# Kernel tuning notes

Hardware: AMD Instinct MI355X
Metric: run time of the kernel (lower is better)

The kernel has to match this reference:

```python
import jax, jax.numpy as jnp
import numpy as np

N_ENTITY = 100000
H_DIM = 512
N_ROWS = 262144
ALPHA = 0.5          # EMA rate for fast state
GATE_TH = 0.5        # gate_threshold buffer
GATE_SCALE = 5.0     # gate_scale buffer
LN_EPS = 1e-5


def setup_inputs() -> dict:
    key = jax.random.key(0)
    k1, k2, k3, k4, k5 = jax.random.split(key, 5)
    entity_emb = jax.random.normal(k1, (N_ROWS, H_DIM), dtype=jnp.float32)
    entity_ids = jax.random.randint(k2, (N_ROWS,), 0, N_ENTITY, dtype=jnp.int64)
    slow_state = 0.1 * jax.random.normal(k3, (N_ENTITY, H_DIM), dtype=jnp.float32)
    fast_state = 0.1 * jax.random.normal(k4, (N_ENTITY, H_DIM), dtype=jnp.float32)
    # torch nn.Linear(2h, h): weight shape (h, 2h), y = x @ W.T + b
    W = jax.random.normal(k5, (H_DIM, 2 * H_DIM), dtype=jnp.float32) * 0.02
    b = jnp.zeros((H_DIM,), dtype=jnp.float32)
    return {"entity_emb": entity_emb, "slow_state": slow_state,
            "fast_state": fast_state, "W": W, "b": b, "entity_ids": entity_ids}


def _layer_norm(x):
    mu = jnp.mean(x, axis=-1, keepdims=True)
    var = jnp.mean(jnp.square(x - mu), axis=-1, keepdims=True)
    return (x - mu) * jax.lax.rsqrt(var + LN_EPS)


def reference(entity_emb, slow_state, fast_state, W, b, entity_ids):
    # ---- fuse_with_state (gate path) ----
    state = slow_state[entity_ids]                                   # (N, h) gather
    is_active = (jnp.sum(jnp.abs(state), axis=-1, keepdims=True) > 1e-6).astype(entity_emb.dtype)
    h_state = _layer_norm(state)
    gate_in = jnp.concatenate([entity_emb, h_state], axis=-1)        # (N, 2h)
    z = jax.nn.sigmoid(gate_in @ W.T + b)                            # (N, h)
    fused = z * entity_emb + (1.0 - z) * h_state
    out = is_active * fused + (1.0 - is_active) * entity_emb

    # ---- writeback (no-grad in torch; scatter-reduce EMA + norm-gated slow update) ----
    ctx = jax.lax.stop_gradient(out)
    ids = entity_ids
    counts = jax.ops.segment_sum(jnp.ones((ctx.shape[0],), ctx.dtype), ids,
                                 num_segments=N_ENTITY)              # (E,)
    ctx_sum = jax.ops.segment_sum(ctx, ids, num_segments=N_ENTITY)   # (E, h)
    ctx_mean = ctx_sum / jnp.clip(counts, 1.0)[:, None]
    touched = (counts > 0)[:, None]
    new_fast_all = (1.0 - ALPHA) * fast_state + ALPHA * ctx_mean
    new_fast = jnp.where(touched, new_fast_all, fast_state)
    diff = new_fast - slow_state
    delta = jnp.linalg.norm(diff, axis=-1, keepdims=True)
    gate = jax.nn.sigmoid(GATE_SCALE * (delta - GATE_TH))
    new_slow = jnp.where(touched, slow_state + gate * diff, slow_state)
    return out, new_fast, new_slow
```

## Files before the change

### kernel.cpp

```cpp
#include <hip/hip_runtime.h>
#include <hip/hip_bf16.h>
#include <cstdint>

#define NROWS 262144
#define HDIM  512
#define NENT  100000
#define SCAN_NBLK ((NENT + 1023) / 1024)

typedef __attribute__((ext_vector_type(4))) float  f32x4;
typedef __attribute__((ext_vector_type(8))) short  bf16x8;
typedef __attribute__((ext_vector_type(4))) short  bf16x4;

static __device__ __forceinline__ unsigned short f2bf(float x) {
    unsigned u = __float_as_uint(x);
    u += 0x7FFF + ((u >> 16) & 1);
    return (unsigned short)(u >> 16);
}
static __device__ __forceinline__ float bf2f(unsigned short h) {
    return __uint_as_float(((unsigned)h) << 16);
}

__global__ void pack_w_kernel(const float* __restrict__ W,
                              unsigned short* __restrict__ WeP,
                              unsigned short* __restrict__ WsP) {
    int g    = blockIdx.x * 256 + threadIdx.x;
    int sel  = g >> 15;
    int gg   = g & 32767;
    int lane = gg & 63;
    int ct   = (gg >> 6) & 3;
    int kt   = (gg >> 8) & 15;
    int w    = gg >> 12;
    int col  = (w * 4 + ct) * 16 + (lane & 15);
    int k    = kt * 32 + ((lane >> 4) << 3) + sel * 512;
    const float* src = W + (size_t)col * 1024 + k;
    f32x4 v0 = *(const f32x4*)(src);
    f32x4 v1 = *(const f32x4*)(src + 4);
    bf16x8 ov;
#pragma unroll
    for (int i = 0; i < 4; ++i) {
        ov[i]     = (short)f2bf(v0[i]);
        ov[4 + i] = (short)f2bf(v1[i]);
    }
    unsigned short* dst = sel ? WsP : WeP;
    *(bf16x8*)(dst + (size_t)gg * 8) = ov;
}

__global__ __launch_bounds__(256) void zero_kernel(unsigned* __restrict__ p) {
    int i = blockIdx.x * 256 + threadIdx.x;
    if (i < NENT) p[i] = 0u;
}

__global__ __launch_bounds__(256) void count_kernel(const int* __restrict__ ids,
                                                    unsigned* __restrict__ counts) {
    int r = blockIdx.x * 256 + threadIdx.x;
    if (r < NROWS) atomicAdd(&counts[ids[r]], 1u);
}

__global__ __launch_bounds__(1024) void scan1_kernel(const unsigned* __restrict__ counts,
                                                     unsigned* __restrict__ off,
                                                     unsigned* __restrict__ bsums) {
    __shared__ unsigned tmp[1024];
    int i = blockIdx.x * 1024 + threadIdx.x;
    unsigned v = (i < NENT) ? counts[i] : 0u;
    tmp[threadIdx.x] = v;
    __syncthreads();
#pragma unroll
    for (int o = 1; o < 1024; o <<= 1) {
        unsigned a = (threadIdx.x >= o) ? tmp[threadIdx.x - o] : 0u;
        __syncthreads();
        tmp[threadIdx.x] += a;
        __syncthreads();
    }
    if (i < NENT) off[i] = tmp[threadIdx.x] - v;
    if (threadIdx.x == 1023) bsums[blockIdx.x] = tmp[1023];
}

__global__ void scan2_kernel(unsigned* __restrict__ bsums) {
    if (threadIdx.x == 0 && blockIdx.x == 0) {
        unsigned s = 0;
        for (int i = 0; i < SCAN_NBLK; ++i) { unsigned t = bsums[i]; bsums[i] = s; s += t; }
    }
}

__global__ __launch_bounds__(1024) void scan3_kernel(unsigned* __restrict__ off,
                                                     const unsigned* __restrict__ bsums,
                                                     unsigned* __restrict__ cursor) {
    int i = blockIdx.x * 1024 + threadIdx.x;
    if (i < NENT) {
        unsigned o = off[i] + bsums[blockIdx.x];
        off[i] = o;
        cursor[i] = o;
    }
    if (i == 0) off[NENT] = NROWS;
}

__global__ __launch_bounds__(256) void fill_kernel(const int* __restrict__ ids,
                                                   unsigned* __restrict__ cursor,
                                                   int* __restrict__ rowidx) {
    int r = blockIdx.x * 256 + threadIdx.x;
    if (r < NROWS) {
        unsigned p = atomicAdd(&cursor[ids[r]], 1u);
        rowidx[p] = r;
    }
}

__global__ __launch_bounds__(512, 4) void entity_kernel(
    const float* __restrict__ slow, const unsigned short* __restrict__ WsP,
    const float* __restrict__ bias, unsigned short* __restrict__ hB,
    unsigned short* __restrict__ GsB, float* __restrict__ actB)
{
    __shared__ unsigned short xLds[2048 * 8];
    __shared__ float muS[32], rsS[32], bS[512];

    const int t    = threadIdx.x;
    const int w    = t >> 6;
    const int lane = t & 63;
    const int brow = blockIdx.x * 32;

    if (t < 128) ((f32x4*)bS)[t] = ((const f32x4*)bias)[t];

    for (int rr = 0; rr < 4; ++rr) {
        int row = w * 4 + rr;
        int e   = brow + row;
        const float* sp = slow + (size_t)e * HDIM;
        f32x4 v0 = ((const f32x4*)sp)[lane * 2];
        f32x4 v1 = ((const f32x4*)sp)[lane * 2 + 1];
        float s = 0.f, s2 = 0.f, sa = 0.f;
#pragma unroll
        for (int i = 0; i < 4; ++i) {
            s  += v0[i] + v1[i];
            s2 += v0[i] * v0[i] + v1[i] * v1[i];
            sa += fabsf(v0[i]) + fabsf(v1[i]);
        }
#pragma unroll
        for (int m = 32; m >= 1; m >>= 1) {
            s  += __shfl_xor(s, m);
            s2 += __shfl_xor(s2, m);
            sa += __shfl_xor(sa, m);
        }
        if (lane == 0) {
            float mu  = s * (1.f / HDIM);
            float var = s2 * (1.f / HDIM) - mu * mu;
            muS[row] = mu;
            rsS[row] = rsqrtf(var + 1e-5f);
            actB[e]  = (sa > 1e-6f) ? 1.f : 0.f;
        }
    }
    __syncthreads();

#pragma unroll
    for (int i = 0; i < 4; ++i) {
        int s  = t + i * 512;
        int T  = s >> 6, ls = s & 63;
        int row = (T & 1) * 16 + (ls & 15);
        int k   = (T >> 1) * 32 + ((ls >> 4) << 3);
        const float* p = slow + (size_t)(brow + row) * HDIM + k;
        f32x4 x0 = *(const f32x4*)p, x1 = *(const f32x4*)(p + 4);
        float mu = muS[row], rs = rsS[row];
        bf16x8 av;
#pragma unroll
        for (int j = 0; j < 4; ++j) {
            av[j]     = (short)f2bf((x0[j] - mu) * rs);
            av[4 + j] = (short)f2bf((x1[j] - mu) * rs);
        }
        ((bf16x8*)xLds)[s] = av;
    }
    __syncthreads();

    f32x4 zero4 = {0.f, 0.f, 0.f, 0.f};
    f32x4 acc[2][4];
#pragma unroll
    for (int i = 0; i < 2; ++i)
#pragma unroll
        for (int j = 0; j < 4; ++j) acc[i][j] = zero4;

    const unsigned short* wpW = WsP + (size_t)w * 32768 + (size_t)lane * 8;

#define LOADW(dst, kt)                                                  \
    {   _Pragma("unroll")                                               \
        for (int ct = 0; ct < 4; ++ct)                                  \
            dst[ct] = *(const bf16x8*)(wpW + ((kt) * 4 + ct) * 512);    \
    }
#define LOADX(dst, kt)                                                  \
    {   _Pragma("unroll")                                               \
        for (int rt = 0; rt < 2; ++rt)                                  \
            dst[rt] = ((const bf16x8*)xLds)[((kt) * 2 + rt) * 64 + lane]; \
    }
#define STEP(wf, xf)                                                    \
    {   _Pragma("unroll")                                               \
        for (int ct = 0; ct < 4; ++ct) {                                \
            acc[0][ct] = __builtin_amdgcn_mfma_f32_16x16x32_bf16(wf[ct], xf[0], acc[0][ct], 0, 0, 0); \
            acc[1][ct] = __builtin_amdgcn_mfma_f32_16x16x32_bf16(wf[ct], xf[1], acc[1][ct], 0, 0, 0); \
        }                                                               \
    }

    {
        bf16x8 wA[4], wB[4], xA[2], xB[2];
        LOADW(wA, 0); LOADX(xA, 0);
#pragma unroll
        for (int kt = 0; kt < 16; kt += 2) {
            if (kt + 1 < 16) { LOADW(wB, kt + 1); LOADX(xB, kt + 1); }
            STEP(wA, xA);
            if (kt + 2 < 16) { LOADW(wA, kt + 2); LOADX(xA, kt + 2); }
            if (kt + 1 < 16) STEP(wB, xB);
        }
    }

#pragma unroll
    for (int rt = 0; rt < 2; ++rt) {
        int e = brow + rt * 16 + (lane & 15);
#pragma unroll
        for (int ct = 0; ct < 4; ++ct) {
            int col0 = w * 64 + ct * 16 + ((lane >> 4) << 2);
            f32x4 bv = *(const f32x4*)&bS[col0];
            bf16x4 gv;
#pragma unroll
            for (int r = 0; r < 4; ++r) gv[r] = (short)f2bf(acc[rt][ct][r] + bv[r]);
            *(bf16x4*)(GsB + (size_t)e * HDIM + col0) = gv;
        }
    }
#pragma unroll
    for (int i = 0; i < 4; ++i) {
        int s  = t + i * 512;
        int T  = s >> 6, ls = s & 63;
        int row = (T & 1) * 16 + (ls & 15);
        int k   = (T >> 1) * 32 + ((ls >> 4) << 3);
        *(bf16x8*)(hB + (size_t)(brow + row) * HDIM + k) = ((const bf16x8*)xLds)[s];
    }
}

__global__ __launch_bounds__(512, 4) void fuse_kernel(
    const float* __restrict__ emb, const unsigned short* __restrict__ WeP,
    const int* __restrict__ ids, const unsigned short* __restrict__ hB,
    const unsigned short* __restrict__ GsB, const float* __restrict__ actB,
    float* __restrict__ out)
{
    __shared__ unsigned short xLds[2048 * 8];
    __shared__ int idS[32];

    const int t    = threadIdx.x;
    const int w    = t >> 6;
    const int lane = t & 63;
    const int brow = blockIdx.x * 32;

    if (t < 32) idS[t] = ids[brow + t];

#pragma unroll
    for (int i = 0; i < 4; ++i) {
        int s  = t + i * 512;
        int T  = s >> 6, ls = s & 63;
        int row = (T & 1) * 16 + (ls & 15);
        int k   = (T >> 1) * 32 + ((ls >> 4) << 3);
        const float* p = emb + (size_t)(brow + row) * HDIM + k;
        f32x4 x0 = *(const f32x4*)p, x1 = *(const f32x4*)(p + 4);
        bf16x8 av;
#pragma unroll
        for (int j = 0; j < 4; ++j) {
            av[j]     = (short)f2bf(x0[j]);
            av[4 + j] = (short)f2bf(x1[j]);
        }
        ((bf16x8*)xLds)[s] = av;
    }
    __syncthreads();

    f32x4 zero4 = {0.f, 0.f, 0.f, 0.f};
    f32x4 acc[2][4];
#pragma unroll
    for (int i = 0; i < 2; ++i)
#pragma unroll
        for (int j = 0; j < 4; ++j) acc[i][j] = zero4;

    const unsigned short* wpW = WeP + (size_t)w * 32768 + (size_t)lane * 8;

    {
        bf16x8 wA[4], wB[4], xA[2], xB[2];
        LOADW(wA, 0); LOADX(xA, 0);
#pragma unroll
        for (int kt = 0; kt < 16; kt += 2) {
            if (kt + 1 < 16) { LOADW(wB, kt + 1); LOADX(xB, kt + 1); }
            STEP(wA, xA);
            if (kt + 2 < 16) { LOADW(wA, kt + 2); LOADX(xA, kt + 2); }
            if (kt + 1 < 16) STEP(wB, xB);
        }
    }
#undef LOADW
#undef LOADX
#undef STEP

#pragma unroll
    for (int rt = 0; rt < 2; ++rt) {
        int rowl = rt * 16 + (lane & 15);
        int grow = brow + rowl;
        int id   = idS[rowl];
        float act = actB[id];
        const unsigned short* gsP = GsB + (size_t)id * HDIM;
        const unsigned short* hP  = hB  + (size_t)id * HDIM;
        float* outP = out + (size_t)grow * HDIM;
#pragma unroll
        for (int ct = 0; ct < 4; ++ct) {
            int col0 = w * 64 + ct * 16 + ((lane >> 4) << 2);
            int Te = ((col0 >> 5) * 2 + rt) * 64 + (((col0 >> 3) & 3) << 4) + (lane & 15);
            const unsigned short* pe = xLds + Te * 8 + (col0 & 7);
            bf16x4 gv = *(const bf16x4*)(gsP + col0);
            bf16x4 hv = *(const bf16x4*)(hP + col0);
            f32x4 o;
#pragma unroll
            for (int r = 0; r < 4; ++r) {
                float ev = bf2f(pe[r]);
                float logit = acc[rt][ct][r] + bf2f(gv[r]);
                float z = 1.f / (1.f + __expf(-logit));
                float fused = z * ev + (1.f - z) * bf2f(hv[r]);
                o[r] = (act > 0.f) ? fused : ev;
            }
            *(f32x4*)(outP + col0) = o;
        }
    }
}

__global__ __launch_bounds__(256) void finalize_kernel(
    const float* __restrict__ fast, const float* __restrict__ slow,
    const float* __restrict__ out, const unsigned* __restrict__ off,
    const int* __restrict__ rowidx, float* __restrict__ nf, float* __restrict__ ns)
{
    int e = blockIdx.x * 4 + (threadIdx.x >> 6);
    if (e >= NENT) return;
    int lane = threadIdx.x & 63;
    size_t base = (size_t)e * HDIM + lane * 8;

    f32x4 f0 = *(const f32x4*)(fast + base), f1 = *(const f32x4*)(fast + base + 4);
    f32x4 l0 = *(const f32x4*)(slow + base), l1 = *(const f32x4*)(slow + base + 4);

    unsigned o0 = off[e], o1 = off[e + 1];
    int c = (int)(o1 - o0);

    if (c == 0) {
        *(f32x4*)(nf + base)     = f0;
        *(f32x4*)(nf + base + 4) = f1;
        *(f32x4*)(ns + base)     = l0;
        *(f32x4*)(ns + base + 4) = l1;
        return;
    }

    f32x4 s0 = {0.f, 0.f, 0.f, 0.f}, s1 = {0.f, 0.f, 0.f, 0.f};
    for (int j = 0; j < c; ++j) {
        int r = rowidx[o0 + j];
        const float* p = out + (size_t)r * HDIM + lane * 8;
        s0 += *(const f32x4*)p;
        s1 += *(const f32x4*)(p + 4);
    }

    float inv = 0.5f / (float)c;
    f32x4 n0, n1, d0, d1;
    float ss = 0.f;
#pragma unroll
    for (int i = 0; i < 4; ++i) {
        n0[i] = 0.5f * f0[i] + s0[i] * inv;
        n1[i] = 0.5f * f1[i] + s1[i] * inv;
        d0[i] = n0[i] - l0[i]; ss += d0[i] * d0[i];
        d1[i] = n1[i] - l1[i]; ss += d1[i] * d1[i];
    }
#pragma unroll
    for (int m = 32; m >= 1; m >>= 1) ss += __shfl_xor(ss, m);
    float delta = sqrtf(ss);
    float gate  = 1.f / (1.f + expf(-5.f * (delta - 0.5f)));

    f32x4 o0v, o1v;
#pragma unroll
    for (int i = 0; i < 4; ++i) {
        o0v[i] = l0[i] + gate * d0[i];
        o1v[i] = l1[i] + gate * d1[i];
    }
    *(f32x4*)(nf + base)     = n0;
    *(f32x4*)(nf + base + 4) = n1;
    *(f32x4*)(ns + base)     = o0v;
    *(f32x4*)(ns + base + 4) = o1v;
}

extern "C" void kernel_launch(void* const* d_in, const int* in_sizes, int n_in,
                              void* d_out, int out_size, void* d_ws, size_t ws_size,
                              hipStream_t stream) {
    const float* emb  = (const float*)d_in[0];
    const float* slow = (const float*)d_in[1];
    const float* fast = (const float*)d_in[2];
    const float* W    = (const float*)d_in[3];
    const float* bias = (const float*)d_in[4];
    const int*   ids  = (const int*)d_in[5];

    float* out = (float*)d_out;
    float* nf  = out + (size_t)NROWS * HDIM;
    float* ns  = nf + (size_t)NENT * HDIM;

    unsigned short* hB  = (unsigned short*)nf;
    unsigned short* GsB = (unsigned short*)ns;

    unsigned short* WeP = (unsigned short*)d_ws;
    unsigned short* WsP = (unsigned short*)((char*)d_ws + (512u << 10));
    float* actB         = (float*)((char*)d_ws + (1024u << 10));
    unsigned* counts    = (unsigned*)((char*)d_ws + (1536u << 10));
    unsigned* off       = (unsigned*)((char*)d_ws + (2048u << 10));
    unsigned* bsums     = (unsigned*)((char*)d_ws + (2560u << 10));
    int*      rowidx    = (int*)((char*)d_ws + (2560u << 10) + 4096);

    zero_kernel<<<(NENT + 255) / 256, 256, 0, stream>>>(counts);
    pack_w_kernel<<<256, 256, 0, stream>>>(W, WeP, WsP);
    entity_kernel<<<NENT / 32, 512, 0, stream>>>(slow, WsP, bias, hB, GsB, actB);
    count_kernel<<<NROWS / 256, 256, 0, stream>>>(ids, counts);
    scan1_kernel<<<SCAN_NBLK, 1024, 0, stream>>>(counts, off, bsums);
    scan2_kernel<<<1, 64, 0, stream>>>(bsums);
    scan3_kernel<<<SCAN_NBLK, 1024, 0, stream>>>(off, bsums, counts);
    fill_kernel<<<NROWS / 256, 256, 0, stream>>>(ids, counts, rowidx);
    fuse_kernel<<<NROWS / 32, 512, 0, stream>>>(emb, WeP, ids, hB, GsB, actB, out);
    finalize_kernel<<<(NENT + 3) / 4, 256, 0, stream>>>(fast, slow, out, off, rowidx, nf, ns);
}
```

Measured before the change: 986.3 us.

## Double fuse_kernel row tile to 64 rows with 16 waves per block

The fuse GEMM block now covers 64 rows using 1024 threads, arranged as 2 row-groups by 8 column-groups of waves, so each weight tile fetched from L2 serves twice as many rows. The packed weight layout changes to be indexed by column tile and k tile, and both the entity and fuse kernels are updated to address it. The goal is to halve weight traffic per output row. The cost is larger LDS use per block and 1024-thread blocks, which may limit occupancy.

```diff
diff --git a/kernel.cpp b/kernel.cpp
--- a/kernel.cpp
+++ b/kernel.cpp
@@ -27,10 +27,9 @@
     int sel  = g >> 15;
     int gg   = g & 32767;
     int lane = gg & 63;
-    int ct   = (gg >> 6) & 3;
-    int kt   = (gg >> 8) & 15;
-    int w    = gg >> 12;
-    int col  = (w * 4 + ct) * 16 + (lane & 15);
+    int kt   = (gg >> 6) & 15;
+    int nt   = gg >> 10;
+    int col  = nt * 16 + (lane & 15);
     int k    = kt * 32 + ((lane >> 4) << 3) + sel * 512;
     const float* src = W + (size_t)col * 1024 + k;
     f32x4 v0 = *(const f32x4*)(src);
@@ -174,14 +173,13 @@
 #pragma unroll
         for (int j = 0; j < 4; ++j) acc[i][j] = zero4;
 
-    const unsigned short* wpW = WsP + (size_t)w * 32768 + (size_t)lane * 8;
-
-#define LOADW(dst, kt)                                                  \
+#define LOADW_A(dst, kt)                                                \
     {   _Pragma("unroll")                                               \
         for (int ct = 0; ct < 4; ++ct)                                  \
-            dst[ct] = *(const bf16x8*)(wpW + ((kt) * 4 + ct) * 512);    \
-    }
-#define LOADX(dst, kt)                                                  \
+            dst[ct] = *(const bf16x8*)(WsP +                            \
+                ((size_t)(((w * 4 + ct) * 16 + (kt)) * 64 + lane) << 3)); \
+    }
+#define LOADX_A(dst, kt)                                                \
     {   _Pragma("unroll")                                               \
         for (int rt = 0; rt < 2; ++rt)                                  \
             dst[rt] = ((const bf16x8*)xLds)[((kt) * 2 + rt) * 64 + lane]; \
@@ -196,15 +194,17 @@
 
     {
         bf16x8 wA[4], wB[4], xA[2], xB[2];
-        LOADW(wA, 0); LOADX(xA, 0);
+        LOADW_A(wA, 0); LOADX_A(xA, 0);
 #pragma unroll
         for (int kt = 0; kt < 16; kt += 2) {
-            if (kt + 1 < 16) { LOADW(wB, kt + 1); LOADX(xB, kt + 1); }
+            if (kt + 1 < 16) { LOADW_A(wB, kt + 1); LOADX_A(xB, kt + 1); }
             STEP(wA, xA);
-            if (kt + 2 < 16) { LOADW(wA, kt + 2); LOADX(xA, kt + 2); }
+            if (kt + 2 < 16) { LOADW_A(wA, kt + 2); LOADX_A(xA, kt + 2); }
             if (kt + 1 < 16) STEP(wB, xB);
         }
     }
+#undef LOADW_A
+#undef LOADX_A
 
 #pragma unroll
     for (int rt = 0; rt < 2; ++rt) {
@@ -229,28 +229,31 @@
     }
 }
 
-__global__ __launch_bounds__(512, 4) void fuse_kernel(
+__global__ __launch_bounds__(1024, 4) void fuse_kernel(
     const float* __restrict__ emb, const unsigned short* __restrict__ WeP,
     const int* __restrict__ ids, const unsigned short* __restrict__ hB,
     const unsigned short* __restrict__ GsB, const float* __restrict__ actB,
     float* __restrict__ out)
 {
-    __shared__ unsigned short xLds[2048 * 8];
-    __shared__ int idS[32];
+    __shared__ unsigned short xLds[4096 * 8];
+    __shared__ int idS[64];
 
     const int t    = threadIdx.x;
     const int w    = t >> 6;
     const int lane = t & 63;
-    const int brow = blockIdx.x * 32;
-
-    if (t < 32) idS[t] = ids[brow + t];
-
-#pragma unroll
-    for (int i = 0; i < 4; ++i) {
-        int s  = t + i * 512;
+    const int wm   = w >> 3;
+    const int wn   = w & 7;
+    const int brow = blockIdx.x * 64;
+
+    if (t < 64) idS[t] = ids[brow + t];
+
+#pragma unroll
+    for (int i = 0; i < 4; ++i) {
+        int s  = t + i * 1024;
         int T  = s >> 6, ls = s & 63;
-        int row = (T & 1) * 16 + (ls & 15);
-        int k   = (T >> 1) * 32 + ((ls >> 4) << 3);
+        int kt  = T >> 2, rt = T & 3;
+        int row = rt * 16 + (ls & 15);
+        int k   = kt * 32 + ((ls >> 4) << 3);
         const float* p = emb + (size_t)(brow + row) * HDIM + k;
         f32x4 x0 = *(const f32x4*)p, x1 = *(const f32x4*)(p + 4);
         bf16x8 av;
@@ -270,26 +273,36 @@
 #pragma unroll
         for (int j = 0; j < 4; ++j) acc[i][j] = zero4;
 
-    const unsigned short* wpW = WeP + (size_t)w * 32768 + (size_t)lane * 8;
+#define LOADW_B(dst, kt)                                                \
+    {   _Pragma("unroll")                                               \
+        for (int ct = 0; ct < 4; ++ct)                                  \
+            dst[ct] = *(const bf16x8*)(WeP +                            \
+                ((size_t)(((wn * 4 + ct) * 16 + (kt)) * 64 + lane) << 3)); \
+    }
+#define LOADX_B(dst, kt)                                                \
+    {   _Pragma("unroll")                                               \
+        for (int rt = 0; rt < 2; ++rt)                                  \
+            dst[rt] = ((const bf16x8*)xLds)[((kt) * 4 + wm * 2 + rt) * 64 + lane]; \
+    }
 
     {
         bf16x8 wA[4], wB[4], xA[2], xB[2];
-        LOADW(wA, 0); LOADX(xA, 0);
+        LOADW_B(wA, 0); LOADX_B(xA, 0);
 #pragma unroll
         for (int kt = 0; kt < 16; kt += 2) {
-            if (kt + 1 < 16) { LOADW(wB, kt + 1); LOADX(xB, kt + 1); }
+            if (kt + 1 < 16) { LOADW_B(wB, kt + 1); LOADX_B(xB, kt + 1); }
             STEP(wA, xA);
-            if (kt + 2 < 16) { LOADW(wA, kt + 2); LOADX(xA, kt + 2); }
+            if (kt + 2 < 16) { LOADW_B(wA, kt + 2); LOADX_B(xA, kt + 2); }
             if (kt + 1 < 16) STEP(wB, xB);
         }
     }
-#undef LOADW
-#undef LOADX
+#undef LOADW_B
+#undef LOADX_B
 #undef STEP
 
 #pragma unroll
     for (int rt = 0; rt < 2; ++rt) {
-        int rowl = rt * 16 + (lane & 15);
+        int rowl = wm * 32 + rt * 16 + (lane & 15);
         int grow = brow + rowl;
         int id   = idS[rowl];
         float act = actB[id];
@@ -298,8 +311,8 @@
         float* outP = out + (size_t)grow * HDIM;
 #pragma unroll
         for (int ct = 0; ct < 4; ++ct) {
-            int col0 = w * 64 + ct * 16 + ((lane >> 4) << 2);
-            int Te = ((col0 >> 5) * 2 + rt) * 64 + (((col0 >> 3) & 3) << 4) + (lane & 15);
+            int col0 = wn * 64 + ct * 16 + ((lane >> 4) << 2);
+            int Te = ((col0 >> 5) * 4 + wm * 2 + rt) * 64 + (((col0 >> 3) & 3) << 4) + (lane & 15);
             const unsigned short* pe = xLds + Te * 8 + (col0 & 7);
             bf16x4 gv = *(const bf16x4*)(gsP + col0);
             bf16x4 hv = *(const bf16x4*)(hP + col0);
@@ -409,6 +422,6 @@
     scan2_kernel<<<1, 64, 0, stream>>>(bsums);
     scan3_kernel<<<SCAN_NBLK, 1024, 0, stream>>>(off, bsums, counts);
     fill_kernel<<<NROWS / 256, 256, 0, stream>>>(ids, counts, rowidx);
-    fuse_kernel<<<NROWS / 32, 512, 0, stream>>>(emb, WeP, ids, hB, GsB, actB, out);
+    fuse_kernel<<<NROWS / 64, 1024, 0, stream>>>(emb, WeP, ids, hB, GsB, actB, out);
     finalize_kernel<<<(NENT + 3) / 4, 256, 0, stream>>>(fast, slow, out, off, rowidx, nf, ns);
 }
```

Result: no change. 974.6 us (-1.2%).
